# Kernel tuning notes

Measured on AMD Instinct MI355X. Metric: run time of the kernel, lower is better.

The kernel has to match this reference:

```python
import jax, jax.numpy as jnp
import numpy as np

EPS = 1e-6
N = 512
D = 8192


def solve_lap_np(cost):
    """Jonker-Volgenant shortest-augmenting-path LAP (same optimum as
    scipy.optimize.linear_sum_assignment). Returns col4row: col assigned to each row."""
    cost = np.asarray(cost, dtype=np.float64)
    n = cost.shape[0]
    u = np.zeros(n)
    v = np.zeros(n)
    path = np.full(n, -1, dtype=np.int64)
    col4row = np.full(n, -1, dtype=np.int64)
    row4col = np.full(n, -1, dtype=np.int64)
    for cur_row in range(n):
        shortest = np.full(n, np.inf)
        SR = np.zeros(n, dtype=bool)  # visited rows
        SC = np.zeros(n, dtype=bool)  # visited cols
        i = cur_row
        min_val = 0.0
        sink = -1
        while sink == -1:
            SR[i] = True
            idx = np.nonzero(~SC)[0]
            r = min_val + cost[i, idx] - u[i] - v[idx]
            upd = r < shortest[idx]
            shortest[idx[upd]] = r[upd]
            path[idx[upd]] = i
            j = idx[np.argmin(shortest[idx])]
            min_val = shortest[j]
            SC[j] = True
            if row4col[j] == -1:
                sink = j
            else:
                i = row4col[j]
        # dual updates
        u[cur_row] += min_val
        sr = np.nonzero(SR)[0]
        sr = sr[sr != cur_row]
        u[sr] += min_val - shortest[col4row[sr]]
        sc = np.nonzero(SC)[0]
        v[sc] -= min_val - shortest[sc]
        # augment along the alternating path
        j = sink
        while True:
            i = path[j]
            row4col[j] = i
            col4row[i], j = j, col4row[i]
            if i == cur_row:
                break
    return col4row


def lap_assign(cost):
    """Optimal assignment as a one-hot labelling matrix (rows -> cols)."""
    n = cost.shape[0]
    col = jax.pure_callback(
        lambda c: solve_lap_np(np.asarray(c)).astype(np.int32),
        jax.ShapeDtypeStruct((n,), jnp.int32),
        cost,
    )
    return jax.nn.one_hot(col, n, dtype=cost.dtype)


def l2_normalize(x):
    # torch F.normalize(p=2, dim=1): x / max(||x||, eps)
    norm = jnp.sqrt(jnp.sum(x * x, axis=1, keepdims=True))
    return x / jnp.maximum(norm, EPS)


def setup_inputs() -> dict:
    key = jax.random.key(0)
    k1, k2, k3 = jax.random.split(key, 3)
    return {
        "un1": jax.random.normal(k1, (N, D), dtype=jnp.float32),
        "un2": jax.random.normal(k2, (N, D), dtype=jnp.float32),
        "un3": jax.random.normal(k3, (N, D), dtype=jnp.float32),
    }


def reference(un1, un2, un3):
    n1 = l2_normalize(un1)
    n2 = l2_normalize(un2)
    n3 = l2_normalize(un3)
    # cosine-distance cost matrices, cycle 1->2->3->1
    c12 = 1.0 - n1 @ n2.T
    c23 = 1.0 - n2 @ n3.T
    c31 = 1.0 - n3 @ n1.T
    x12 = lap_assign(c12)
    x23 = lap_assign(c23)
    x31 = lap_assign(c31)
    return (x12, x23, x31)
```

## Files before the change

kernel.cpp:

```cpp
#include <hip/hip_runtime.h>
#include <math.h>

#define NN 512
#define DD 8192

__global__ __launch_bounds__(256) void norm_kernel(
    const float* __restrict__ a0, const float* __restrict__ a1,
    const float* __restrict__ a2, float* __restrict__ scales) {
  const float* mats[3] = {a0, a1, a2};
  const int m = blockIdx.y;
  const int row = blockIdx.x;
  const float* x = mats[m] + (size_t)row * DD;
  const int tid = threadIdx.x;
  float s = 0.f;
  for (int k = tid * 4; k < DD; k += 256 * 4) {
    const float4 v = *(const float4*)(x + k);
    s += v.x * v.x + v.y * v.y + v.z * v.z + v.w * v.w;
  }
#pragma unroll
  for (int off = 32; off > 0; off >>= 1) s += __shfl_down(s, off);
  __shared__ float ws[4];
  if ((tid & 63) == 0) ws[tid >> 6] = s;
  __syncthreads();
  if (tid == 0) {
    const float t = ws[0] + ws[1] + ws[2] + ws[3];
    scales[m * NN + row] = 1.0f / fmaxf(sqrtf(t), 1e-6f);
  }
}

__global__ __launch_bounds__(256) void cost_gemm_kernel(
    const float* __restrict__ a0, const float* __restrict__ a1,
    const float* __restrict__ a2, const float* __restrict__ scales,
    float* __restrict__ cost_all) {
  const float* mats[3] = {a0, a1, a2};
  const int p = blockIdx.z;
  const int pA = p, pB = (p + 1) % 3;
  const float* A = mats[pA];
  const float* B = mats[pB];
  float* C = cost_all + (size_t)p * NN * NN;

  __shared__ float lds_a[64 * 64];
  __shared__ float lds_b[64 * 64];

  const int tid = threadIdx.x;
  const int rowBase = blockIdx.y * 64;
  const int colBase = blockIdx.x * 64;

  const int lr = tid & 63;
  const int lq = tid >> 6;

  const float* Arow = A + (size_t)(rowBase + lr) * DD;
  const float* Brow = B + (size_t)(colBase + lr) * DD;

  float acc[4][4];
#pragma unroll
  for (int i = 0; i < 4; ++i)
#pragma unroll
    for (int j = 0; j < 4; ++j) acc[i][j] = 0.f;

  const int tx = tid & 15, ty = tid >> 4;

  for (int kb = 0; kb < DD; kb += 64) {
#pragma unroll
    for (int qq = 0; qq < 4; ++qq) {
      const int q = lq + qq * 4;
      const float4 av = *(const float4*)(Arow + kb + q * 4);
      const float4 bv = *(const float4*)(Brow + kb + q * 4);
      lds_a[(q * 4 + 0) * 64 + lr] = av.x;
      lds_a[(q * 4 + 1) * 64 + lr] = av.y;
      lds_a[(q * 4 + 2) * 64 + lr] = av.z;
      lds_a[(q * 4 + 3) * 64 + lr] = av.w;
      lds_b[(q * 4 + 0) * 64 + lr] = bv.x;
      lds_b[(q * 4 + 1) * 64 + lr] = bv.y;
      lds_b[(q * 4 + 2) * 64 + lr] = bv.z;
      lds_b[(q * 4 + 3) * 64 + lr] = bv.w;
    }
    __syncthreads();
#pragma unroll 8
    for (int k = 0; k < 64; ++k) {
      const float4 a4 = *(const float4*)(&lds_a[k * 64 + ty * 4]);
      const float4 b4 = *(const float4*)(&lds_b[k * 64 + tx * 4]);
      const float as0[4] = {a4.x, a4.y, a4.z, a4.w};
      const float bs0[4] = {b4.x, b4.y, b4.z, b4.w};
#pragma unroll
      for (int ii = 0; ii < 4; ++ii)
#pragma unroll
        for (int jj = 0; jj < 4; ++jj)
          acc[ii][jj] = fmaf(as0[ii], bs0[jj], acc[ii][jj]);
    }
    __syncthreads();
  }

#pragma unroll
  for (int ii = 0; ii < 4; ++ii) {
    const int gr = rowBase + ty * 4 + ii;
    const float sa = scales[pA * NN + gr];
#pragma unroll
    for (int jj = 0; jj < 4; ++jj) {
      const int gc = colBase + tx * 4 + jj;
      const float sb = scales[pB * NN + gc];
      C[gr * NN + gc] = 1.0f - acc[ii][jj] * sa * sb;
    }
  }
}


__device__ __forceinline__ int SW(int c) { return ((c & 7) << 6) | (c >> 3); }

__device__ __forceinline__ unsigned wave_min_u32(unsigned x) {
  int t;
  t = __builtin_amdgcn_update_dpp((int)x, (int)x, 0x111, 0xf, 0xf, false);
  x = ((unsigned)t < x) ? (unsigned)t : x;
  t = __builtin_amdgcn_update_dpp((int)x, (int)x, 0x112, 0xf, 0xf, false);
  x = ((unsigned)t < x) ? (unsigned)t : x;
  t = __builtin_amdgcn_update_dpp((int)x, (int)x, 0x114, 0xf, 0xf, false);
  x = ((unsigned)t < x) ? (unsigned)t : x;
  t = __builtin_amdgcn_update_dpp((int)x, (int)x, 0x118, 0xf, 0xf, false);
  x = ((unsigned)t < x) ? (unsigned)t : x;
  t = __builtin_amdgcn_update_dpp((int)x, (int)x, 0x142, 0xf, 0xf, false);
  x = ((unsigned)t < x) ? (unsigned)t : x;
  t = __builtin_amdgcn_update_dpp((int)x, (int)x, 0x143, 0xf, 0xf, false);
  x = ((unsigned)t < x) ? (unsigned)t : x;
  return (unsigned)__builtin_amdgcn_readlane((int)x, 63);
}

__device__ __forceinline__ double readlane_f64(double x, int lane) {
  const long long b = __double_as_longlong(x);
  const int lo = __builtin_amdgcn_readlane((int)(b & 0xffffffffLL), lane);
  const int hi = __builtin_amdgcn_readlane((int)(b >> 32), lane);
  return __longlong_as_double(((long long)hi << 32) | (unsigned long long)(unsigned)lo);
}

__device__ __forceinline__ unsigned long long f64key(double x) {
  const long long b = __double_as_longlong(x);
  return (b < 0) ? ~(unsigned long long)b
                 : ((unsigned long long)b | 0x8000000000000000ULL);
}

__global__ __launch_bounds__(64) void lap_kernel(
    const float* __restrict__ cost_all, float* __restrict__ out) {
  const int p = blockIdx.x;
  const float* cost = cost_all + (size_t)p * NN * NN;
  float* outp = out + (size_t)p * NN * NN;
  const int tid = threadIdx.x;

  __shared__ double sh_u[NN];
  __shared__ double sh_shortest[NN];
  __shared__ int sh_path[NN];
  __shared__ int sh_x[NN];
  __shared__ int sh_y[NN];

  const double INF = __builtin_inf();

#pragma unroll
  for (int q = 0; q < 8; ++q) {
    const int e = tid * 8 + q;
    sh_x[SW(e)] = -1;
    sh_y[SW(e)] = -1;
    sh_u[SW(e)] = 0.0;
  }
  double myV[8];
#pragma unroll
  for (int q = 0; q < 8; ++q) myV[q] = 0.0;
  __syncthreads();

  for (int cur_row = 0; cur_row < NN; ++cur_row) {
    double selv[8];
    double vAdj[8];
    double frz[8];
    int myPath[8];
    unsigned pl[8];
#pragma unroll
    for (int q = 0; q < 8; ++q) {
      selv[q] = INF;
      vAdj[q] = myV[q];
      frz[q] = 0.0;
      myPath[q] = 0;
    }
#pragma unroll
    for (int q = 0; q < 8; ++q)
      pl[q] = ((unsigned)q << 10) | (unsigned)(sh_y[SW(tid * 8 + q)] + 1);

    unsigned scMask = 0, srMask = 0;
    int i = cur_row;
    double minv = 0.0;
    int sink = -1;
    int pendQ = -1, pendLane = 0;

    while (true) {
      const float4 c0 = *(const float4*)(cost + (size_t)i * NN + tid * 8);
      const float4 c1 = *(const float4*)(cost + (size_t)i * NN + tid * 8 + 4);
      const double u_i = sh_u[SW(i)];
      if ((i >> 3) == tid) srMask |= 1u << (i & 7);
      if (pendQ >= 0) {
        const bool me = (tid == pendLane);
#define APPLY_SC(K)                                                     \
        if (pendQ == K) {                                               \
          if (me) {                                                     \
            selv[K] = INF; vAdj[K] = -INF; frz[K] = minv;               \
            scMask |= 1u << K;                                          \
          }                                                             \
        }
        APPLY_SC(0) APPLY_SC(1) APPLY_SC(2) APPLY_SC(3)
        APPLY_SC(4) APPLY_SC(5) APPLY_SC(6) APPLY_SC(7)
#undef APPLY_SC
      }
      const double mu = minv - u_i;
      double base[8];
#pragma unroll
      for (int q = 0; q < 8; ++q) base[q] = mu - vAdj[q];
      const float cf[8] = {c0.x, c0.y, c0.z, c0.w, c1.x, c1.y, c1.z, c1.w};
#pragma unroll
      for (int q = 0; q < 8; ++q) {
        const double r = (double)cf[q] + base[q];
        const bool cnd = r < selv[q];
        selv[q] = fmin(selv[q], r);
        myPath[q] = cnd ? i : myPath[q];
      }
      const bool t01 = selv[1] < selv[0];
      double v01 = t01 ? selv[1] : selv[0]; unsigned p01 = t01 ? pl[1] : pl[0];
      const bool t23 = selv[3] < selv[2];
      double v23 = t23 ? selv[3] : selv[2]; unsigned p23 = t23 ? pl[3] : pl[2];
      const bool t45 = selv[5] < selv[4];
      double v45 = t45 ? selv[5] : selv[4]; unsigned p45 = t45 ? pl[5] : pl[4];
      const bool t67 = selv[7] < selv[6];
      double v67 = t67 ? selv[7] : selv[6]; unsigned p67 = t67 ? pl[7] : pl[6];
      const bool ta = v23 < v01;
      const double vab = ta ? v23 : v01; const unsigned pab = ta ? p23 : p01;
      const bool tb = v67 < v45;
      const double vcd = tb ? v67 : v45; const unsigned pcd = tb ? p67 : p45;
      const bool tc = vcd < vab;
      const double lv = tc ? vcd : vab; const unsigned lp = tc ? pcd : pab;
      const unsigned long long kk = f64key(lv);
      const unsigned hi = (unsigned)(kk >> 32);
      const unsigned lo = (unsigned)kk;
      const unsigned minhi = wave_min_u32(hi);
      unsigned long long bal = __ballot(hi == minhi);
      int srcLane;
      if (__popcll(bal) == 1) {
        srcLane = __ffsll(bal) - 1;
      } else {
        const unsigned lo2 = (hi == minhi) ? lo : 0xFFFFFFFFu;
        const unsigned minlo = wave_min_u32(lo2);
        bal = __ballot((hi == minhi) && (lo == minlo));
        srcLane = __ffsll(bal) - 1;
      }
      const unsigned pw = (unsigned)__builtin_amdgcn_readlane((int)lp, srcLane);
      const int qb = (int)(pw >> 10);
      const int r4 = (int)(pw & 0x3FFu) - 1;
      minv = readlane_f64(lv, srcLane);
      if (r4 < 0) {
        sink = srcLane * 8 + qb;
        break;
      }
      i = r4;
      pendQ = qb;
      pendLane = srcLane;
    }

#pragma unroll
    for (int q = 0; q < 8; ++q) {
      sh_shortest[SW(tid * 8 + q)] = frz[q];
      sh_path[SW(tid * 8 + q)] = myPath[q];
    }
    __syncthreads();
#pragma unroll
    for (int q = 0; q < 8; ++q) {
      const int row = tid * 8 + q;
      if (row == cur_row) {
        sh_u[SW(row)] += minv;
      } else if (srMask & (1u << q)) {
        sh_u[SW(row)] += minv - sh_shortest[SW(sh_x[SW(row)])];
      }
      if (scMask & (1u << q)) myV[q] -= minv - frz[q];
    }
    __syncthreads();
    if (tid == 0) {
      int j = sink;
      while (true) {
        const int pi = sh_path[SW(j)];
        sh_y[SW(j)] = pi;
        const int tmp = sh_x[SW(pi)];
        sh_x[SW(pi)] = j;
        j = tmp;
        if (pi == cur_row) break;
      }
    }
    __syncthreads();
  }

#pragma unroll
  for (int q = 0; q < 8; ++q) {
    const int row = tid * 8 + q;
    outp[(size_t)row * NN + sh_x[SW(row)]] = 1.0f;
  }
}

extern "C" void kernel_launch(void* const* d_in, const int* in_sizes, int n_in,
                              void* d_out, int out_size, void* d_ws, size_t ws_size,
                              hipStream_t stream) {
  const float* un1 = (const float*)d_in[0];
  const float* un2 = (const float*)d_in[1];
  const float* un3 = (const float*)d_in[2];
  float* out = (float*)d_out;

  float* cost = (float*)d_ws;
  float* scales = cost + (size_t)3 * NN * NN;

  hipMemsetAsync(d_out, 0, (size_t)out_size * sizeof(float), stream);

  norm_kernel<<<dim3(NN, 3), 256, 0, stream>>>(un1, un2, un3, scales);
  cost_gemm_kernel<<<dim3(NN / 64, NN / 64, 3), 256, 0, stream>>>(un1, un2, un3, scales, cost);
  lap_kernel<<<3, 64, 0, stream>>>(cost, out);
}
```

Measured before the change: 5.883 ms.

## Defer shortest-path updates in LAP loop to shorten the serial critical path

The LAP inner loop no longer folds the new reduced costs into selv before the wave argmin. It reduces the fresh row costs and the previous selv separately with two local trees, merges the two winners, and applies the selv and path updates lazily at the start of the next iteration. This takes the per-element update off the dependency chain between the cost load and the cross-lane minimum, at the price of extra registers and a second local tree. The cost GEMM's K tile also shrinks from 64 to 32 with a full unroll, halving LDS use at the cost of more barriers.

Result: slower. 6.100 ms (+3.7%).

```diff
diff --git a/kernel.cpp b/kernel.cpp
--- a/kernel.cpp
+++ b/kernel.cpp
@@ -39,8 +39,8 @@
   const float* B = mats[pB];
   float* C = cost_all + (size_t)p * NN * NN;
 
-  __shared__ float lds_a[64 * 64];
-  __shared__ float lds_b[64 * 64];
+  __shared__ float lds_a[32 * 64];
+  __shared__ float lds_b[32 * 64];
 
   const int tid = threadIdx.x;
   const int rowBase = blockIdx.y * 64;
@@ -60,9 +60,9 @@
 
   const int tx = tid & 15, ty = tid >> 4;
 
-  for (int kb = 0; kb < DD; kb += 64) {
-#pragma unroll
-    for (int qq = 0; qq < 4; ++qq) {
+  for (int kb = 0; kb < DD; kb += 32) {
+#pragma unroll
+    for (int qq = 0; qq < 2; ++qq) {
       const int q = lq + qq * 4;
       const float4 av = *(const float4*)(Arow + kb + q * 4);
       const float4 bv = *(const float4*)(Brow + kb + q * 4);
@@ -76,8 +76,8 @@
       lds_b[(q * 4 + 3) * 64 + lr] = bv.w;
     }
     __syncthreads();
-#pragma unroll 8
-    for (int k = 0; k < 64; ++k) {
+#pragma unroll
+    for (int k = 0; k < 32; ++k) {
       const float4 a4 = *(const float4*)(&lds_a[k * 64 + ty * 4]);
       const float4 b4 = *(const float4*)(&lds_b[k * 64 + tx * 4]);
       const float as0[4] = {a4.x, a4.y, a4.z, a4.w};
@@ -136,6 +136,31 @@
   return (b < 0) ? ~(unsigned long long)b
                  : ((unsigned long long)b | 0x8000000000000000ULL);
 }
+
+#define TREE8(v, pq, oV, oP)                                                   \
+  do {                                                                         \
+    const bool t01 = (v)[1] < (v)[0];                                          \
+    const double a0 = t01 ? (v)[1] : (v)[0];                                   \
+    const unsigned b0 = t01 ? (pq)[1] : (pq)[0];                               \
+    const bool t23 = (v)[3] < (v)[2];                                          \
+    const double a1 = t23 ? (v)[3] : (v)[2];                                   \
+    const unsigned b1 = t23 ? (pq)[3] : (pq)[2];                               \
+    const bool t45 = (v)[5] < (v)[4];                                          \
+    const double a2 = t45 ? (v)[5] : (v)[4];                                   \
+    const unsigned b2 = t45 ? (pq)[5] : (pq)[4];                               \
+    const bool t67 = (v)[7] < (v)[6];                                          \
+    const double a3 = t67 ? (v)[7] : (v)[6];                                   \
+    const unsigned b3 = t67 ? (pq)[7] : (pq)[6];                               \
+    const bool ta = a1 < a0;                                                   \
+    const double c0_ = ta ? a1 : a0;                                           \
+    const unsigned d0_ = ta ? b1 : b0;                                         \
+    const bool tb = a3 < a2;                                                   \
+    const double c1_ = tb ? a3 : a2;                                           \
+    const unsigned d1_ = tb ? b3 : b2;                                         \
+    const bool tc = c1_ < c0_;                                                 \
+    (oV) = tc ? c1_ : c0_;                                                     \
+    (oP) = tc ? d1_ : d0_;                                                     \
+  } while (0)
 
 __global__ __launch_bounds__(64) void lap_kernel(
     const float* __restrict__ cost_all, float* __restrict__ out) {
@@ -168,6 +193,7 @@
     double selv[8];
     double vAdj[8];
     double frz[8];
+    double rPrev[8];
     int myPath[8];
     unsigned pl[8];
 #pragma unroll
@@ -175,6 +201,7 @@
       selv[q] = INF;
       vAdj[q] = myV[q];
       frz[q] = 0.0;
+      rPrev[q] = INF;
       myPath[q] = 0;
     }
 #pragma unroll
@@ -184,14 +211,25 @@
     unsigned scMask = 0, srMask = 0;
     int i = cur_row;
     double minv = 0.0;
+    double lvW = 0.0;
+    int srcL = 0;
+    int iPrev = 0;
+    int pendQ = -1, pendLane = 0;
     int sink = -1;
-    int pendQ = -1, pendLane = 0;
 
     while (true) {
       const float4 c0 = *(const float4*)(cost + (size_t)i * NN + tid * 8);
       const float4 c1 = *(const float4*)(cost + (size_t)i * NN + tid * 8 + 4);
       const double u_i = sh_u[SW(i)];
       if ((i >> 3) == tid) srMask |= 1u << (i & 7);
+
+      minv = readlane_f64(lvW, srcL);
+#pragma unroll
+      for (int q = 0; q < 8; ++q) {
+        const bool cnd = rPrev[q] < selv[q];
+        myPath[q] = cnd ? iPrev : myPath[q];
+        selv[q] = fmin(selv[q], rPrev[q]);
+      }
       if (pendQ >= 0) {
         const bool me = (tid == pendLane);
 #define APPLY_SC(K)                                                     \
@@ -205,33 +243,26 @@
         APPLY_SC(4) APPLY_SC(5) APPLY_SC(6) APPLY_SC(7)
 #undef APPLY_SC
       }
+      double oV;
+      unsigned oP;
+      TREE8(selv, pl, oV, oP);
       const double mu = minv - u_i;
       double base[8];
 #pragma unroll
       for (int q = 0; q < 8; ++q) base[q] = mu - vAdj[q];
+
       const float cf[8] = {c0.x, c0.y, c0.z, c0.w, c1.x, c1.y, c1.z, c1.w};
 #pragma unroll
-      for (int q = 0; q < 8; ++q) {
-        const double r = (double)cf[q] + base[q];
-        const bool cnd = r < selv[q];
-        selv[q] = fmin(selv[q], r);
-        myPath[q] = cnd ? i : myPath[q];
-      }
-      const bool t01 = selv[1] < selv[0];
-      double v01 = t01 ? selv[1] : selv[0]; unsigned p01 = t01 ? pl[1] : pl[0];
-      const bool t23 = selv[3] < selv[2];
-      double v23 = t23 ? selv[3] : selv[2]; unsigned p23 = t23 ? pl[3] : pl[2];
-      const bool t45 = selv[5] < selv[4];
-      double v45 = t45 ? selv[5] : selv[4]; unsigned p45 = t45 ? pl[5] : pl[4];
-      const bool t67 = selv[7] < selv[6];
-      double v67 = t67 ? selv[7] : selv[6]; unsigned p67 = t67 ? pl[7] : pl[6];
-      const bool ta = v23 < v01;
-      const double vab = ta ? v23 : v01; const unsigned pab = ta ? p23 : p01;
-      const bool tb = v67 < v45;
-      const double vcd = tb ? v67 : v45; const unsigned pcd = tb ? p67 : p45;
-      const bool tc = vcd < vab;
-      const double lv = tc ? vcd : vab; const unsigned lp = tc ? pcd : pab;
-      const unsigned long long kk = f64key(lv);
+      for (int q = 0; q < 8; ++q) rPrev[q] = (double)cf[q] + base[q];
+      double rV;
+      unsigned rP;
+      TREE8(rPrev, pl, rV, rP);
+      const bool rlt = rV < oV;
+      const bool olt = oV < rV;
+      const double wV = rlt ? rV : oV;
+      const unsigned pmin = (oP < rP) ? oP : rP;
+      const unsigned wP = rlt ? rP : (olt ? oP : pmin);
+      const unsigned long long kk = f64key(wV);
       const unsigned hi = (unsigned)(kk >> 32);
       const unsigned lo = (unsigned)kk;
       const unsigned minhi = wave_min_u32(hi);
@@ -245,17 +276,40 @@
         bal = __ballot((hi == minhi) && (lo == minlo));
         srcLane = __ffsll(bal) - 1;
       }
-      const unsigned pw = (unsigned)__builtin_amdgcn_readlane((int)lp, srcLane);
+      const unsigned pw = (unsigned)__builtin_amdgcn_readlane((int)wP, srcLane);
       const int qb = (int)(pw >> 10);
       const int r4 = (int)(pw & 0x3FFu) - 1;
-      minv = readlane_f64(lv, srcLane);
+      lvW = wV;
+      srcL = srcLane;
+      iPrev = i;
+      pendQ = qb;
+      pendLane = srcLane;
       if (r4 < 0) {
         sink = srcLane * 8 + qb;
         break;
       }
       i = r4;
-      pendQ = qb;
-      pendLane = srcLane;
+    }
+
+    minv = readlane_f64(lvW, srcL);
+#pragma unroll
+    for (int q = 0; q < 8; ++q) {
+      const bool cnd = rPrev[q] < selv[q];
+      myPath[q] = cnd ? iPrev : myPath[q];
+      selv[q] = fmin(selv[q], rPrev[q]);
+    }
+    {
+      const bool me = (tid == pendLane);
+#define APPLY_SC(K)                                                     \
+      if (pendQ == K) {                                                 \
+        if (me) {                                                       \
+          selv[K] = INF; vAdj[K] = -INF; frz[K] = minv;                 \
+          scMask |= 1u << K;                                            \
+        }                                                               \
+      }
+      APPLY_SC(0) APPLY_SC(1) APPLY_SC(2) APPLY_SC(3)
+      APPLY_SC(4) APPLY_SC(5) APPLY_SC(6) APPLY_SC(7)
+#undef APPLY_SC
     }
 
 #pragma unroll
```
